# Kernel tuning notes

Hardware: AMD Instinct MI355X
Metric: run time of the kernel (lower is better)

## Reference

```python
import jax, jax.numpy as jnp
import numpy as np

IN_CH, OUT_CH, KS = 64, 128, 3
GRID, DEG = 8, 3
STRIDE, PAD = 1, 1
SIZE = IN_CH * KS * KS            # 576
NCOEF = GRID + DEG                # 11
GRID_RANGE = (-1.0, 1.0)


def _xavier_uniform(key, shape):
    fan_out, fan_in = shape
    a = float(np.sqrt(6.0 / (fan_in + fan_out)))
    return jax.random.uniform(key, shape, minval=-a, maxval=a, dtype=jnp.float32)


def setup_inputs() -> dict:
    key = jax.random.key(0)
    k1, k2, k3 = jax.random.split(key, 3)
    x = jax.random.normal(k1, (8, IN_CH, 32, 32), dtype=jnp.float32)
    # non-trainable knot grid, one row per unfolded feature
    knots = jnp.tile(jnp.linspace(GRID_RANGE[0], GRID_RANGE[1], GRID + 1, dtype=jnp.float32)[None, :], (SIZE, 1))
    coeff = 0.1 * jax.random.normal(k2, (OUT_CH, SIZE, NCOEF), dtype=jnp.float32)
    base_weights = _xavier_uniform(k3, (OUT_CH, SIZE))
    spline_weights = jnp.ones((OUT_CH, SIZE), dtype=jnp.float32)
    return {"x": x, "knots": knots, "coeff": coeff,
            "base_weights": base_weights, "spline_weights": spline_weights}


def bspline_basis(x, grid, k):
    # x: (S, P) evaluation points; grid: (S, G+1) knots. Returns (S, G+k, P).
    h = (grid[:, -1:] - grid[:, :1]) / (grid.shape[1] - 1)
    left = grid[:, :1] - h * jnp.arange(k, 0, -1, dtype=x.dtype)
    right = grid[:, -1:] + h * jnp.arange(1, k + 1, dtype=x.dtype)
    g = jnp.concatenate([left, grid, right], axis=1)  # (S, G+1+2k)
    xe = x[:, None, :]
    B = ((xe >= g[:, :-1, None]) & (xe < g[:, 1:, None])).astype(x.dtype)
    for d in range(1, k + 1):  # de Boor recursion over fixed degree
        B = ((xe - g[:, :-(d + 1), None]) / (g[:, d:-1, None] - g[:, :-(d + 1), None]) * B[:, :-1]
             + (g[:, d + 1:, None] - xe) / (g[:, d + 1:, None] - g[:, 1:-d, None]) * B[:, 1:])
    return B


def _unfold(x):
    # torch F.unfold with channel-major (c, kh, kw) feature ordering
    N, C, H, W = x.shape
    xp = jnp.pad(x, ((0, 0), (0, 0), (PAD, PAD), (PAD, PAD)))
    Hp = (H + 2 * PAD - KS) // STRIDE + 1
    Wp = (W + 2 * PAD - KS) // STRIDE + 1
    patches = jnp.stack([xp[:, :, i:i + STRIDE * Hp:STRIDE, j:j + STRIDE * Wp:STRIDE]
                         for i in range(KS) for j in range(KS)], axis=2)  # (N, C, KS*KS, Hp, Wp)
    L = Hp * Wp
    u = patches.reshape(N, SIZE, L)              # (N, size, L)
    u = jnp.transpose(u, (1, 0, 2)).reshape(SIZE, N * L)  # (size, N*L), col = n*L + l
    return u, Hp, Wp


def reference(x, knots, coeff, base_weights, spline_weights):
    N = x.shape[0]
    u, Hp, Wp = _unfold(x)                                   # (size, P)
    base = base_weights @ jax.nn.silu(u)                     # (Cout, P)
    B = bspline_basis(u, knots, DEG)                         # (size, ncoef, P)
    eff = spline_weights[:, :, None] * coeff                 # (Cout, size, ncoef)
    spl = jnp.einsum('csj,sjp->cp', eff, B)                  # (Cout, P)
    out = (base + spl).reshape(OUT_CH, N, Hp, Wp)
    return jnp.transpose(out, (1, 0, 2, 3))                  # (N, Cout, Hp, Wp)
```

## Files before the change

kernel.cpp:

```cpp
#include <hip/hip_runtime.h>


typedef __attribute__((ext_vector_type(8))) short bf16x8;
typedef __attribute__((ext_vector_type(4))) float f32x4;
typedef __attribute__((ext_vector_type(16))) float f32x16;
typedef __attribute__((ext_vector_type(4))) unsigned short u16x4;

#define WSWZ_BYTES 1769472
#define PART_OFF   WSWZ_BYTES

__device__ __forceinline__ short f2bf(float f) {
    union { float f; unsigned u; } c; c.f = f;
    unsigned r = c.u + 0x7fffu + ((c.u >> 16) & 1u);
    return (short)(r >> 16);
}
__device__ __forceinline__ float bf2f(unsigned short u) {
    union { unsigned u; float f; } c; c.u = ((unsigned)u) << 16;
    return c.f;
}

__global__ void kan_weights(const float* __restrict__ coeff,
                            const float* __restrict__ basew,
                            const float* __restrict__ splw,
                            short* __restrict__ Wswz) {
    __shared__ float coeffL[6336];
    __shared__ float basewL[576];
    __shared__ float splwL[576];
    const int co = blockIdx.x;
    const int t  = threadIdx.x;
    const float* crow = coeff + co * 6336;
    for (int i = t; i < 6336; i += 256) coeffL[i] = crow[i];
    for (int i = t; i < 576; i += 256) {
        basewL[i] = basew[co * 576 + i];
        splwL[i]  = splw[co * 576 + i];
    }
    __syncthreads();
    const int cb = co >> 5, lm = co & 31;
    for (int c = t; c < 864; c += 256) {
        int kk16 = c >> 1, kh = c & 1;
        int f  = kk16 / 36;
        int rm = kk16 - f * 36;
        int tap = rm >> 2, q = rm & 3;
        bf16x8 pack;
#pragma unroll
        for (int j = 0; j < 8; ++j) {
            int ci = q * 16 + kh * 8 + j;
            int s  = ci * 9 + tap;
            float v = (f == 0) ? basewL[s] : splwL[s] * coeffL[s * 11 + (f - 1)];
            pack[j] = f2bf(v);
        }
        *(bf16x8*)(Wswz + (size_t)((kk16 * 4 + cb) * 64 + kh * 32 + lm) * 8) = pack;
    }
}

__global__ __launch_bounds__(256, 2)
void kan_gemm(const float* __restrict__ x,
              const short* __restrict__ Wswz,
              float* __restrict__ part) {
    __shared__ unsigned short xs[4 * 64 * 36];
    __shared__ short Bs[3 * 8704];

    const int t  = threadIdx.x;
    const int w  = t >> 6;
    const int l  = t & 63;
    const int ln = l & 31;
    const int kh = l >> 5;

    const int bz    = blockIdx.x;
    const int fg    = bz & 3;
    const int ptile = bz >> 2;
    const int n     = ptile >> 4;
    const int y0    = (ptile & 15) << 1;

#pragma unroll
    for (int it = 0; it < 8; ++it) {
        int cg = t + it * 256;
        int rr = cg >> 9, ci = (cg >> 3) & 63, q = cg & 7;
        int y  = y0 - 1 + rr;
        f32x4 v = {0.f, 0.f, 0.f, 0.f};
        if (y >= 0 && y < 32)
            v = *(const f32x4*)(x + (((n * 64 + ci) * 32 + y) * 32 + q * 4));
        u16x4 p;
        p.x = (unsigned short)f2bf(v.x); p.y = (unsigned short)f2bf(v.y);
        p.z = (unsigned short)f2bf(v.z); p.w = (unsigned short)f2bf(v.w);
        *(u16x4*)&xs[(rr * 64 + ci) * 36 + q * 4] = p;
    }
    __syncthreads();

    const int f0 = fg * 3;
    for (int it = t; it < 1088; it += 256) {
        int rr  = it / 272;
        int rem = it - rr * 272;
        int xp = rem >> 3, cch = rem & 7, c0 = cch << 3;
        bool interior = (xp >= 1 && xp <= 32);
        bf16x8 packs[3];
#pragma unroll
        for (int j = 0; j < 8; ++j) {
            float v = interior ? bf2f(xs[(rr * 64 + c0 + j) * 36 + (xp - 1)]) : 0.f;
            float silu = v / (1.f + __expf(-v));
            float tt = 4.f * v + 7.f;
            int   i0 = -100;
            float b0 = 0.f, b1 = 0.f, b2 = 0.f, b3 = 0.f;
            if (tt >= 0.f && tt < 14.f) {
                i0 = (int)tt;
                float fr  = tt - (float)i0;
                float omf = 1.f - fr;
                float fr2 = fr * fr, fr3 = fr2 * fr;
                b0 = omf * omf * omf * (1.f / 6.f);
                b1 = (3.f * fr3 - 6.f * fr2 + 4.f) * (1.f / 6.f);
                b2 = (-3.f * fr3 + 3.f * fr2 + 3.f * fr + 1.f) * (1.f / 6.f);
                b3 = fr3 * (1.f / 6.f);
            }
#pragma unroll
            for (int p = 0; p < 3; ++p) {
                int f = f0 + p;
                float val;
                if (f == 0) val = silu;
                else {
                    int jj = f - 1;
                    val = 0.f;
                    val = (jj == i0 - 3) ? b0 : val;
                    val = (jj == i0 - 2) ? b1 : val;
                    val = (jj == i0 - 1) ? b2 : val;
                    val = (jj == i0    ) ? b3 : val;
                }
                packs[p][j] = f2bf(val);
            }
        }
        int pix = rr * 34 + xp;
        int swz = (cch ^ (pix & 7)) << 3;
#pragma unroll
        for (int p = 0; p < 3; ++p)
            *(bf16x8*)&Bs[p * 8704 + pix * 64 + swz] = packs[p];
    }
    __syncthreads();

    f32x16 acc[2];
#pragma unroll
    for (int pb = 0; pb < 2; ++pb)
#pragma unroll
        for (int r = 0; r < 16; ++r)
            acc[pb][r] = 0.f;

    const short* Abase = Wswz + (size_t)w * 512 + (size_t)l * 8;
#pragma unroll 1
    for (int p = 0; p < 3; ++p) {
        const short* B0 = Bs + p * 8704;
        const int kbase = (f0 + p) * 36;
#pragma unroll
        for (int rm = 0; rm < 36; ++rm) {
            const int tap = rm >> 2, q = rm & 3;
            const int dy  = tap / 3;
            const int dx  = tap - dy * 3;
            bf16x8 a = *(const bf16x8*)(Abase + (size_t)(kbase + rm) * 2048);
            const int c = q * 2 + kh;
#pragma unroll
            for (int pb = 0; pb < 2; ++pb) {
                int pix = (pb + dy) * 34 + ln + dx;
                bf16x8 b = *(const bf16x8*)&B0[pix * 64 + ((c ^ (pix & 7)) << 3)];
                acc[pb] = __builtin_amdgcn_mfma_f32_32x32x16_bf16(a, b, acc[pb], 0, 0, 0);
            }
        }
    }

    float* dst = part + (size_t)fg * 1048576;
#pragma unroll
    for (int pb = 0; pb < 2; ++pb) {
        int y = y0 + pb;
#pragma unroll
        for (int r = 0; r < 16; ++r) {
            int row = (r & 3) + 8 * (r >> 2) + 4 * kh;
            int co  = w * 32 + row;
            dst[((size_t)(n * 128 + co) * 32 + y) * 32 + ln] = acc[pb][r];
        }
    }
}

__global__ void kan_reduce(const float* __restrict__ part,
                           float* __restrict__ out) {
    int g = blockIdx.x * 256 + threadIdx.x;
    f32x4 a = ((const f32x4*)part)[g];
#pragma unroll
    for (int s = 1; s < 4; ++s)
        a += ((const f32x4*)(part + (size_t)s * 1048576))[g];
    ((f32x4*)out)[g] = a;
}

extern "C" void kernel_launch(void* const* d_in, const int* in_sizes, int n_in,
                              void* d_out, int out_size, void* d_ws, size_t ws_size,
                              hipStream_t stream) {
    const float* x     = (const float*)d_in[0];
    const float* coeff = (const float*)d_in[2];
    const float* basew = (const float*)d_in[3];
    const float* splw  = (const float*)d_in[4];
    float* out = (float*)d_out;

    short* Wswz = (short*)d_ws;
    float* part = (float*)((char*)d_ws + PART_OFF);

    kan_weights<<<128, 256, 0, stream>>>(coeff, basew, splw, Wswz);
    kan_gemm<<<512, 256, 0, stream>>>(x, Wswz, part);
    kan_reduce<<<1024, 256, 0, stream>>>(part, out);
}
```

Before: 106.9 us.

## Double-buffer B-tile feature builds and raise occupancy to four blocks per CU

Replaces the three-slab B tile in shared memory with a two-slab ring. Each feature slab is built just before it is consumed, overlapping the basis computation for the next feature with the MFMA loop on the current one. This cuts LDS usage enough to raise launch bounds to four blocks per SM, and shrinks the xs row pitch from 36 to 34. The cost is an extra barrier per feature step, recomputing the basis terms for each feature separately rather than once per input value, and a tighter register budget.

```diff
diff --git a/kernel.cpp b/kernel.cpp
--- a/kernel.cpp
+++ b/kernel.cpp
@@ -53,12 +53,12 @@
     }
 }
 
-__global__ __launch_bounds__(256, 2)
+__global__ __launch_bounds__(256, 4)
 void kan_gemm(const float* __restrict__ x,
               const short* __restrict__ Wswz,
               float* __restrict__ part) {
-    __shared__ unsigned short xs[4 * 64 * 36];
-    __shared__ short Bs[3 * 8704];
+    __shared__ unsigned short xs[4 * 64 * 34];
+    __shared__ short Bs[2][8704];
 
     const int t  = threadIdx.x;
     const int w  = t >> 6;
@@ -71,6 +71,7 @@
     const int ptile = bz >> 2;
     const int n     = ptile >> 4;
     const int y0    = (ptile & 15) << 1;
+    const int f0    = fg * 3;
 
 #pragma unroll
     for (int it = 0; it < 8; ++it) {
@@ -83,40 +84,39 @@
         u16x4 p;
         p.x = (unsigned short)f2bf(v.x); p.y = (unsigned short)f2bf(v.y);
         p.z = (unsigned short)f2bf(v.z); p.w = (unsigned short)f2bf(v.w);
-        *(u16x4*)&xs[(rr * 64 + ci) * 36 + q * 4] = p;
+        *(u16x4*)&xs[(rr * 64 + ci) * 34 + q * 4] = p;
     }
     __syncthreads();
 
-    const int f0 = fg * 3;
-    for (int it = t; it < 1088; it += 256) {
-        int rr  = it / 272;
-        int rem = it - rr * 272;
-        int xp = rem >> 3, cch = rem & 7, c0 = cch << 3;
-        bool interior = (xp >= 1 && xp <= 32);
-        bf16x8 packs[3];
-#pragma unroll
-        for (int j = 0; j < 8; ++j) {
-            float v = interior ? bf2f(xs[(rr * 64 + c0 + j) * 36 + (xp - 1)]) : 0.f;
-            float silu = v / (1.f + __expf(-v));
-            float tt = 4.f * v + 7.f;
-            int   i0 = -100;
-            float b0 = 0.f, b1 = 0.f, b2 = 0.f, b3 = 0.f;
-            if (tt >= 0.f && tt < 14.f) {
-                i0 = (int)tt;
-                float fr  = tt - (float)i0;
-                float omf = 1.f - fr;
-                float fr2 = fr * fr, fr3 = fr2 * fr;
-                b0 = omf * omf * omf * (1.f / 6.f);
-                b1 = (3.f * fr3 - 6.f * fr2 + 4.f) * (1.f / 6.f);
-                b2 = (-3.f * fr3 + 3.f * fr2 + 3.f * fr + 1.f) * (1.f / 6.f);
-                b3 = fr3 * (1.f / 6.f);
-            }
-#pragma unroll
-            for (int p = 0; p < 3; ++p) {
-                int f = f0 + p;
+    auto buildB = [&](int f, int buf) {
+        short* B = Bs[buf];
+        for (int it = t; it < 1088; it += 256) {
+            int rr  = it / 272;
+            int rem = it - rr * 272;
+            int xp = rem >> 3, cch = rem & 7, c0 = cch << 3;
+            bool interior = (xp >= 1 && xp <= 32);
+            int xcol = interior ? (xp - 1) : 0;
+            bf16x8 pack;
+#pragma unroll
+            for (int j = 0; j < 8; ++j) {
+                float v = interior ? bf2f(xs[(rr * 64 + c0 + j) * 34 + xcol]) : 0.f;
                 float val;
-                if (f == 0) val = silu;
-                else {
+                if (f == 0) {
+                    val = v / (1.f + __expf(-v));
+                } else {
+                    float tt = 4.f * v + 7.f;
+                    int   i0 = -100;
+                    float b0 = 0.f, b1 = 0.f, b2 = 0.f, b3 = 0.f;
+                    if (tt >= 0.f && tt < 14.f) {
+                        i0 = (int)tt;
+                        float fr  = tt - (float)i0;
+                        float omf = 1.f - fr;
+                        float fr2 = fr * fr, fr3 = fr2 * fr;
+                        b0 = omf * omf * omf * (1.f / 6.f);
+                        b1 = (3.f * fr3 - 6.f * fr2 + 4.f) * (1.f / 6.f);
+                        b2 = (-3.f * fr3 + 3.f * fr2 + 3.f * fr + 1.f) * (1.f / 6.f);
+                        b3 = fr3 * (1.f / 6.f);
+                    }
                     int jj = f - 1;
                     val = 0.f;
                     val = (jj == i0 - 3) ? b0 : val;
@@ -124,15 +124,14 @@
                     val = (jj == i0 - 1) ? b2 : val;
                     val = (jj == i0    ) ? b3 : val;
                 }
-                packs[p][j] = f2bf(val);
+                pack[j] = f2bf(val);
             }
-        }
-        int pix = rr * 34 + xp;
-        int swz = (cch ^ (pix & 7)) << 3;
-#pragma unroll
-        for (int p = 0; p < 3; ++p)
-            *(bf16x8*)&Bs[p * 8704 + pix * 64 + swz] = packs[p];
-    }
+            int pix = rr * 34 + xp;
+            *(bf16x8*)&B[pix * 64 + ((cch ^ (pix & 7)) << 3)] = pack;
+        }
+    };
+
+    buildB(f0, 0);
     __syncthreads();
 
     f32x16 acc[2];
@@ -143,9 +142,12 @@
             acc[pb][r] = 0.f;
 
     const short* Abase = Wswz + (size_t)w * 512 + (size_t)l * 8;
+
 #pragma unroll 1
     for (int p = 0; p < 3; ++p) {
-        const short* B0 = Bs + p * 8704;
+        if (p < 2) buildB(f0 + p + 1, (p + 1) & 1);
+
+        const short* B0 = Bs[p & 1];
         const int kbase = (f0 + p) * 36;
 #pragma unroll
         for (int rm = 0; rm < 36; ++rm) {
@@ -161,6 +163,7 @@
                 acc[pb] = __builtin_amdgcn_mfma_f32_32x32x16_bf16(a, b, acc[pb], 0, 0, 0);
             }
         }
+        __syncthreads();
     }
 
     float* dst = part + (size_t)fg * 1048576;
```

Result: slower. 124.2 us (+16.2%).
